# Kernel optimization log

Measured on AMD Instinct MI355X. Metric: run time of the kernel, lower is better.

## Reference

```python
import jax, jax.numpy as jnp
import numpy as np

BATCH = 256
SEQ = 2048        # sequences (in_features of each per-channel Linear)
C = 32            # input_size (number of independent channels/layers)
EMB = 2048        # embedding_dim (out_features)


def setup_inputs() -> dict:
    key = jax.random.key(0)
    kx, kw, kb = jax.random.split(key, 3)
    x = jax.random.normal(kx, (BATCH, SEQ, C), dtype=jnp.float32)
    # PyTorch nn.Linear init: U(-1/sqrt(fan_in), 1/sqrt(fan_in))
    bound = 1.0 / np.sqrt(SEQ)
    W = jax.random.uniform(kw, (C, SEQ, EMB), minval=-bound, maxval=bound, dtype=jnp.float32)
    b = jax.random.uniform(kb, (C, EMB), minval=-bound, maxval=bound, dtype=jnp.float32)
    return {"x": x, "W": W, "b": b}


def reference(x, W, b):
    # x: (B, S, C) -> transpose to (B, C, S); per-channel Linear + ReLU.
    # Grouped GEMM: out[b,c,e] = relu(sum_s x[b,s,c] * W[c,s,e] + b[c,e])
    xc = jnp.transpose(x, (0, 2, 1))                 # (B, C, S)
    out = jnp.einsum('bcs,cse->bce', xc, W) + b      # (B, C, E)
    return jax.nn.relu(out)
```

## Files before the change

kernel.cpp:

```cpp
#include <hip/hip_runtime.h>

#define BATCH 256
#define SEQ   2048
#define NC    32
#define EMB   2048
#define NT    32

typedef unsigned short ushort_t;
using f32x4  = __attribute__((ext_vector_type(4))) float;
using bf16x8 = __attribute__((ext_vector_type(8))) short;

using u32_gl = __attribute__((address_space(1))) const unsigned int;
using u32_ld = __attribute__((address_space(3))) unsigned int;

__device__ __forceinline__ unsigned short f2bf(float f) {
  unsigned int u = __float_as_uint(f);
  u += 0x7FFFu + ((u >> 16) & 1u);
  return (unsigned short)(u >> 16);
}

__global__ __launch_bounds__(256) void transpose_x_kernel(
    const float* __restrict__ x, ushort_t* __restrict__ xT) {
  __shared__ float tile[64][33];
  const int b  = blockIdx.x >> 5;
  const int st = blockIdx.x & 31;
  const int t  = threadIdx.x;
  const float* src = x + ((size_t)b * SEQ + (size_t)st * 64) * NC;
#pragma unroll
  for (int i = 0; i < 2; ++i) {
    int idx = t + i * 256;
    float4 v = reinterpret_cast<const float4*>(src)[idx];
    int s = idx >> 3;
    int c = (idx & 7) * 4;
    tile[s][c + 0] = v.x; tile[s][c + 1] = v.y;
    tile[s][c + 2] = v.z; tile[s][c + 3] = v.w;
  }
  __syncthreads();
  const int c  = t >> 3;
  const int si = (t & 7) * 8;
  unsigned int q[4];
#pragma unroll
  for (int p = 0; p < 4; ++p) {
    unsigned int h0 = f2bf(tile[si + 2 * p + 0][c]);
    unsigned int h1 = f2bf(tile[si + 2 * p + 1][c]);
    q[p] = h0 | (h1 << 16);
  }
  ushort_t* dst = xT + (size_t)c * (BATCH * SEQ) + (size_t)b * SEQ + st * 64 + si;
  *reinterpret_cast<uint4*>(dst) = make_uint4(q[0], q[1], q[2], q[3]);
}

template <int P>
__device__ __forceinline__ void gemm_iter(
    int t, const ushort_t* __restrict__ xTc, const float* __restrict__ Wc,
    char* AldsB, char* BldsB, f32x4 (&wv)[2][4], f32x4 (&acc)[4][4],
    int tid, int wr, int wc, int g, int lm, int e0) {
  const int srow4 = tid >> 5;
  const int e4    = tid & 31;

  asm volatile("s_waitcnt vmcnt(4)" ::: "memory");
#pragma unroll
  for (int i = 0; i < 4; ++i) {
    const int e_local = e4 * 4 + i;
    unsigned int q0 = (unsigned)f2bf(wv[P][0][i]) | ((unsigned)f2bf(wv[P][1][i]) << 16);
    unsigned int q1 = (unsigned)f2bf(wv[P][2][i]) | ((unsigned)f2bf(wv[P][3][i]) << 16);
    int byte = (e_local * 128 + srow4 * 8) ^ ((e_local & 7) << 4);
    *reinterpret_cast<uint2*>(BldsB + P * 16384 + byte) = make_uint2(q0, q1);
  }

  {
    const int tn = (t + 1) & (NT - 1);
    const float* wp = Wc + (size_t)(tn * 64 + srow4 * 4) * EMB + e0 + e4 * 4;
#pragma unroll
    for (int r = 0; r < 4; ++r)
      wv[P ^ 1][r] = *reinterpret_cast<const f32x4*>(wp + (size_t)r * EMB);
  }

  asm volatile("s_waitcnt lgkmcnt(0)" ::: "memory");
  __builtin_amdgcn_s_barrier();

  {
    const int s0n = ((t + 1) & (NT - 1)) * 64;
#pragma unroll
    for (int i = 0; i < 4; ++i) {
      int ch   = i * 512 + tid;
      int m    = ch >> 3;
      int slot = (ch & 7) ^ (m & 7);
      const ushort_t* src = xTc + (size_t)m * SEQ + s0n + slot * 8;
      __builtin_amdgcn_global_load_lds(
          (u32_gl*)src, (u32_ld*)(AldsB + (P ^ 1) * 32768 + ch * 16), 16, 0, 0);
    }
  }

  asm volatile("s_waitcnt vmcnt(8)" ::: "memory");
  __builtin_amdgcn_sched_barrier(0);

  __builtin_amdgcn_s_barrier();

#pragma unroll
  for (int ks = 0; ks < 2; ++ks) {
    bf16x8 af[4], bfr[4];
#pragma unroll
    for (int mi = 0; mi < 4; ++mi) {
      int m_local = wr * 64 + mi * 16 + lm;
      int byte = (m_local * 128 + (ks * 4 + g) * 16) ^ ((m_local & 7) << 4);
      af[mi] = *reinterpret_cast<const bf16x8*>(AldsB + P * 32768 + byte);
    }
#pragma unroll
    for (int ni = 0; ni < 4; ++ni) {
      int e_local = wc * 64 + ni * 16 + lm;
      int byte = (e_local * 128 + (ks * 4 + g) * 16) ^ ((e_local & 7) << 4);
      bfr[ni] = *reinterpret_cast<const bf16x8*>(BldsB + P * 16384 + byte);
    }
#pragma unroll
    for (int mi = 0; mi < 4; ++mi)
#pragma unroll
      for (int ni = 0; ni < 4; ++ni)
        acc[mi][ni] = __builtin_amdgcn_mfma_f32_16x16x32_bf16(
            af[mi], bfr[ni], acc[mi][ni], 0, 0, 0);
  }
}

__global__ __launch_bounds__(512, 2) void grouped_gemm_pipe(
    const ushort_t* __restrict__ xT,
    const float* __restrict__ W,
    const float* __restrict__ bias,
    float* __restrict__ out) {
  __shared__ ushort_t Alds[2][256 * 64];
  __shared__ ushort_t Blds[2][128 * 64];

  const int bid = (blockIdx.x & 7) * 64 + (blockIdx.x >> 3);
  const int c   = bid >> 4;
  const int et  = bid & 15;
  const int e0  = et * 128;

  const int tid  = threadIdx.x;
  const int w    = tid >> 6;
  const int wr   = w >> 1;
  const int wc   = w & 1;
  const int lane = tid & 63;
  const int g    = lane >> 4;
  const int lm   = lane & 15;

  const float* Wc = W + (size_t)c * SEQ * EMB;
  const ushort_t* xTc = xT + (size_t)c * (BATCH * SEQ);
  char* AldsB = (char*)&Alds[0][0];
  char* BldsB = (char*)&Blds[0][0];

  f32x4 wv[2][4];
  f32x4 acc[4][4];
#pragma unroll
  for (int i = 0; i < 4; ++i)
#pragma unroll
    for (int j = 0; j < 4; ++j) acc[i][j] = (f32x4){0.f, 0.f, 0.f, 0.f};

  {
    const int srow4 = tid >> 5;
    const int e4    = tid & 31;
    const float* wp = Wc + (size_t)(srow4 * 4) * EMB + e0 + e4 * 4;
#pragma unroll
    for (int r = 0; r < 4; ++r)
      wv[0][r] = *reinterpret_cast<const f32x4*>(wp + (size_t)r * EMB);
#pragma unroll
    for (int i = 0; i < 4; ++i) {
      int ch   = i * 512 + tid;
      int m    = ch >> 3;
      int slot = (ch & 7) ^ (m & 7);
      const ushort_t* src = xTc + (size_t)m * SEQ + slot * 8;
      __builtin_amdgcn_global_load_lds(
          (u32_gl*)src, (u32_ld*)(AldsB + ch * 16), 16, 0, 0);
    }
  }

  for (int t = 0; t < NT; t += 2) {
    gemm_iter<0>(t,     xTc, Wc, AldsB, BldsB, wv, acc, tid, wr, wc, g, lm, e0);
    gemm_iter<1>(t + 1, xTc, Wc, AldsB, BldsB, wv, acc, tid, wr, wc, g, lm, e0);
  }

  asm volatile("s_waitcnt vmcnt(0)" ::: "memory");

  const float* bc = bias + (size_t)c * EMB;
#pragma unroll
  for (int ni = 0; ni < 4; ++ni) {
    const int e = e0 + wc * 64 + ni * 16 + lm;
    const float bv = bc[e];
#pragma unroll
    for (int mi = 0; mi < 4; ++mi) {
      f32x4 a = acc[mi][ni];
      const int mbase = wr * 64 + mi * 16 + g * 4;
#pragma unroll
      for (int r = 0; r < 4; ++r) {
        float v = a[r] + bv;
        v = fmaxf(v, 0.f);
        out[((size_t)(mbase + r) * NC + c) * EMB + e] = v;
      }
    }
  }
}

__global__ __launch_bounds__(256, 2) void grouped_gemm_fallback(
    const float* __restrict__ x, const float* __restrict__ W,
    const float* __restrict__ bias, float* __restrict__ out) {
  __shared__ ushort_t Alds[128 * 64];
  __shared__ ushort_t Blds[128 * 64];
  const int bid = blockIdx.x;
  const int c   = bid >> 5;
  const int et  = (bid >> 1) & 15;
  const int bt  = bid & 1;
  const int b0  = bt * 128;
  const int e0  = et * 128;
  const int tid  = threadIdx.x;
  const int w    = tid >> 6;
  const int wr   = w >> 1;
  const int wc   = w & 1;
  const int lane = tid & 63;
  const int g    = lane >> 4;
  const int lm   = lane & 15;
  const float* Wc = W + (size_t)c * SEQ * EMB;
  const int srow8 = tid >> 5;
  const int e4    = tid & 31;
  f32x4 acc[4][4];
#pragma unroll
  for (int i = 0; i < 4; ++i)
#pragma unroll
    for (int j = 0; j < 4; ++j) acc[i][j] = (f32x4){0.f, 0.f, 0.f, 0.f};
  for (int s0 = 0; s0 < SEQ; s0 += 64) {
#pragma unroll
    for (int i = 0; i < 4; ++i) {
      int ch   = i * 256 + tid;
      int m    = ch >> 3;
      int slot = (ch & 7) ^ (m & 7);
      const float* src = x + (size_t)(b0 + m) * (SEQ * NC)
                           + (size_t)(s0 + slot * 8) * NC + c;
      unsigned int q[4];
#pragma unroll
      for (int p = 0; p < 4; ++p) {
        unsigned int h0 = f2bf(src[(2 * p + 0) * NC]);
        unsigned int h1 = f2bf(src[(2 * p + 1) * NC]);
        q[p] = h0 | (h1 << 16);
      }
      *reinterpret_cast<uint4*>((char*)&Alds[0] + ch * 16) =
          make_uint4(q[0], q[1], q[2], q[3]);
    }
    {
      const float* wp = Wc + (size_t)(s0 + srow8 * 8) * EMB + e0 + e4 * 4;
      f32x4 wvv[8];
#pragma unroll
      for (int r = 0; r < 8; ++r)
        wvv[r] = *reinterpret_cast<const f32x4*>(wp + (size_t)r * EMB);
#pragma unroll
      for (int i = 0; i < 4; ++i) {
        const int e_local = e4 * 4 + i;
        unsigned int q0 = (unsigned)f2bf(wvv[0][i]) | ((unsigned)f2bf(wvv[1][i]) << 16);
        unsigned int q1 = (unsigned)f2bf(wvv[2][i]) | ((unsigned)f2bf(wvv[3][i]) << 16);
        unsigned int q2 = (unsigned)f2bf(wvv[4][i]) | ((unsigned)f2bf(wvv[5][i]) << 16);
        unsigned int q3 = (unsigned)f2bf(wvv[6][i]) | ((unsigned)f2bf(wvv[7][i]) << 16);
        int byte = (e_local * 128 + srow8 * 16) ^ ((e_local & 7) << 4);
        *reinterpret_cast<uint4*>((char*)&Blds[0] + byte) =
            make_uint4(q0, q1, q2, q3);
      }
    }
    __syncthreads();
#pragma unroll
    for (int ks = 0; ks < 2; ++ks) {
      bf16x8 af[4], bfr[4];
#pragma unroll
      for (int mi = 0; mi < 4; ++mi) {
        int m_local = wr * 64 + mi * 16 + lm;
        int byte = (m_local * 128 + (ks * 4 + g) * 16) ^ ((m_local & 7) << 4);
        af[mi] = *reinterpret_cast<const bf16x8*>((const char*)&Alds[0] + byte);
      }
#pragma unroll
      for (int ni = 0; ni < 4; ++ni) {
        int e_local = wc * 64 + ni * 16 + lm;
        int byte = (e_local * 128 + (ks * 4 + g) * 16) ^ ((e_local & 7) << 4);
        bfr[ni] = *reinterpret_cast<const bf16x8*>((const char*)&Blds[0] + byte);
      }
#pragma unroll
      for (int mi = 0; mi < 4; ++mi)
#pragma unroll
        for (int ni = 0; ni < 4; ++ni)
          acc[mi][ni] = __builtin_amdgcn_mfma_f32_16x16x32_bf16(
              af[mi], bfr[ni], acc[mi][ni], 0, 0, 0);
    }
    __syncthreads();
  }
  const float* bc = bias + (size_t)c * EMB;
#pragma unroll
  for (int ni = 0; ni < 4; ++ni) {
    const int e = e0 + wc * 64 + ni * 16 + lm;
    const float bv = bc[e];
#pragma unroll
    for (int mi = 0; mi < 4; ++mi) {
      f32x4 a = acc[mi][ni];
      const int mbase = b0 + wr * 64 + mi * 16 + g * 4;
#pragma unroll
      for (int r = 0; r < 4; ++r) {
        float v = a[r] + bv;
        v = fmaxf(v, 0.f);
        out[((size_t)(mbase + r) * NC + c) * EMB + e] = v;
      }
    }
  }
}

extern "C" void kernel_launch(void* const* d_in, const int* in_sizes, int n_in,
                              void* d_out, int out_size, void* d_ws, size_t ws_size,
                              hipStream_t stream) {
  const float* x    = (const float*)d_in[0];
  const float* W    = (const float*)d_in[1];
  const float* bias = (const float*)d_in[2];
  float* out        = (float*)d_out;

  const size_t xT_bytes = (size_t)NC * BATCH * SEQ * sizeof(ushort_t);

  if (ws_size >= xT_bytes) {
    ushort_t* xT = (ushort_t*)d_ws;
    transpose_x_kernel<<<BATCH * (SEQ / 64), 256, 0, stream>>>(x, xT);
    grouped_gemm_pipe<<<NC * (EMB / 128), 512, 0, stream>>>(xT, W, bias, out);
  } else {
    grouped_gemm_fallback<<<NC * 2 * (EMB / 128), 256, 0, stream>>>(x, W, bias, out);
  }
}
```

Before: 158.5 us.

## Shrink GEMM tile to 256x64 with 4 waves and reorder W conversion after prefetch

The pipelined grouped GEMM now uses 64-wide E tiles with 256 threads (4 waves each covering 64 rows) instead of 128-wide tiles with 512 threads. This doubles the block count to 1024 and shrinks B LDS. The W fp32->bf16 conversion and LDS store now run after the next W prefetch is issued, with the waitcnt thresholds adjusted to match. In exchange, each block reloads the full 256x64 A tile for only half as many output columns, which doubles A traffic per FLOP.

```diff
diff --git a/kernel.cpp b/kernel.cpp
--- a/kernel.cpp
+++ b/kernel.cpp
@@ -13,10 +13,10 @@
 using u32_gl = __attribute__((address_space(1))) const unsigned int;
 using u32_ld = __attribute__((address_space(3))) unsigned int;
 
-__device__ __forceinline__ unsigned short f2bf(float f) {
+__device__ __forceinline__ unsigned int f2bf(float f) {
   unsigned int u = __float_as_uint(f);
   u += 0x7FFFu + ((u >> 16) & 1u);
-  return (unsigned short)(u >> 16);
+  return u >> 16;
 }
 
 __global__ __launch_bounds__(256) void transpose_x_kernel(
@@ -53,19 +53,9 @@
 __device__ __forceinline__ void gemm_iter(
     int t, const ushort_t* __restrict__ xTc, const float* __restrict__ Wc,
     char* AldsB, char* BldsB, f32x4 (&wv)[2][4], f32x4 (&acc)[4][4],
-    int tid, int wr, int wc, int g, int lm, int e0) {
-  const int srow4 = tid >> 5;
-  const int e4    = tid & 31;
-
-  asm volatile("s_waitcnt vmcnt(4)" ::: "memory");
-#pragma unroll
-  for (int i = 0; i < 4; ++i) {
-    const int e_local = e4 * 4 + i;
-    unsigned int q0 = (unsigned)f2bf(wv[P][0][i]) | ((unsigned)f2bf(wv[P][1][i]) << 16);
-    unsigned int q1 = (unsigned)f2bf(wv[P][2][i]) | ((unsigned)f2bf(wv[P][3][i]) << 16);
-    int byte = (e_local * 128 + srow4 * 8) ^ ((e_local & 7) << 4);
-    *reinterpret_cast<uint2*>(BldsB + P * 16384 + byte) = make_uint2(q0, q1);
-  }
+    int tid, int wr, int g, int lm, int e0) {
+  const int srow4 = tid >> 4;
+  const int e4    = tid & 15;
 
   {
     const int tn = (t + 1) & (NT - 1);
@@ -75,14 +65,24 @@
       wv[P ^ 1][r] = *reinterpret_cast<const f32x4*>(wp + (size_t)r * EMB);
   }
 
+  asm volatile("s_waitcnt vmcnt(12)" ::: "memory");
+#pragma unroll
+  for (int i = 0; i < 4; ++i) {
+    const int e_local = e4 * 4 + i;
+    unsigned int q0 = f2bf(wv[P][0][i]) | (f2bf(wv[P][1][i]) << 16);
+    unsigned int q1 = f2bf(wv[P][2][i]) | (f2bf(wv[P][3][i]) << 16);
+    int byte = (e_local * 128 + srow4 * 8) ^ ((e_local & 7) << 4);
+    *reinterpret_cast<uint2*>(BldsB + P * 8192 + byte) = make_uint2(q0, q1);
+  }
+
   asm volatile("s_waitcnt lgkmcnt(0)" ::: "memory");
   __builtin_amdgcn_s_barrier();
 
   {
     const int s0n = ((t + 1) & (NT - 1)) * 64;
 #pragma unroll
-    for (int i = 0; i < 4; ++i) {
-      int ch   = i * 512 + tid;
+    for (int i = 0; i < 8; ++i) {
+      int ch   = i * 256 + tid;
       int m    = ch >> 3;
       int slot = (ch & 7) ^ (m & 7);
       const ushort_t* src = xTc + (size_t)m * SEQ + s0n + slot * 8;
@@ -91,7 +91,7 @@
     }
   }
 
-  asm volatile("s_waitcnt vmcnt(8)" ::: "memory");
+  asm volatile("s_waitcnt vmcnt(12)" ::: "memory");
   __builtin_amdgcn_sched_barrier(0);
 
   __builtin_amdgcn_s_barrier();
@@ -107,9 +107,9 @@
     }
 #pragma unroll
     for (int ni = 0; ni < 4; ++ni) {
-      int e_local = wc * 64 + ni * 16 + lm;
+      int e_local = ni * 16 + lm;
       int byte = (e_local * 128 + (ks * 4 + g) * 16) ^ ((e_local & 7) << 4);
-      bfr[ni] = *reinterpret_cast<const bf16x8*>(BldsB + P * 16384 + byte);
+      bfr[ni] = *reinterpret_cast<const bf16x8*>(BldsB + P * 8192 + byte);
     }
 #pragma unroll
     for (int mi = 0; mi < 4; ++mi)
@@ -120,23 +120,21 @@
   }
 }
 
-__global__ __launch_bounds__(512, 2) void grouped_gemm_pipe(
+__global__ __launch_bounds__(256, 2) void grouped_gemm_pipe(
     const ushort_t* __restrict__ xT,
     const float* __restrict__ W,
     const float* __restrict__ bias,
     float* __restrict__ out) {
   __shared__ ushort_t Alds[2][256 * 64];
-  __shared__ ushort_t Blds[2][128 * 64];
-
-  const int bid = (blockIdx.x & 7) * 64 + (blockIdx.x >> 3);
-  const int c   = bid >> 4;
-  const int et  = bid & 15;
-  const int e0  = et * 128;
+  __shared__ ushort_t Blds[2][64 * 64];
+
+  const int bid = (blockIdx.x & 7) * 128 + (blockIdx.x >> 3);
+  const int c   = bid >> 5;
+  const int et  = bid & 31;
+  const int e0  = et * 64;
 
   const int tid  = threadIdx.x;
-  const int w    = tid >> 6;
-  const int wr   = w >> 1;
-  const int wc   = w & 1;
+  const int wr   = tid >> 6;
   const int lane = tid & 63;
   const int g    = lane >> 4;
   const int lm   = lane & 15;
@@ -154,15 +152,15 @@
     for (int j = 0; j < 4; ++j) acc[i][j] = (f32x4){0.f, 0.f, 0.f, 0.f};
 
   {
-    const int srow4 = tid >> 5;
-    const int e4    = tid & 31;
+    const int srow4 = tid >> 4;
+    const int e4    = tid & 15;
     const float* wp = Wc + (size_t)(srow4 * 4) * EMB + e0 + e4 * 4;
 #pragma unroll
     for (int r = 0; r < 4; ++r)
       wv[0][r] = *reinterpret_cast<const f32x4*>(wp + (size_t)r * EMB);
 #pragma unroll
-    for (int i = 0; i < 4; ++i) {
-      int ch   = i * 512 + tid;
+    for (int i = 0; i < 8; ++i) {
+      int ch   = i * 256 + tid;
       int m    = ch >> 3;
       int slot = (ch & 7) ^ (m & 7);
       const ushort_t* src = xTc + (size_t)m * SEQ + slot * 8;
@@ -172,8 +170,8 @@
   }
 
   for (int t = 0; t < NT; t += 2) {
-    gemm_iter<0>(t,     xTc, Wc, AldsB, BldsB, wv, acc, tid, wr, wc, g, lm, e0);
-    gemm_iter<1>(t + 1, xTc, Wc, AldsB, BldsB, wv, acc, tid, wr, wc, g, lm, e0);
+    gemm_iter<0>(t,     xTc, Wc, AldsB, BldsB, wv, acc, tid, wr, g, lm, e0);
+    gemm_iter<1>(t + 1, xTc, Wc, AldsB, BldsB, wv, acc, tid, wr, g, lm, e0);
   }
 
   asm volatile("s_waitcnt vmcnt(0)" ::: "memory");
@@ -181,7 +179,7 @@
   const float* bc = bias + (size_t)c * EMB;
 #pragma unroll
   for (int ni = 0; ni < 4; ++ni) {
-    const int e = e0 + wc * 64 + ni * 16 + lm;
+    const int e = e0 + ni * 16 + lm;
     const float bv = bc[e];
 #pragma unroll
     for (int mi = 0; mi < 4; ++mi) {
@@ -250,10 +248,10 @@
 #pragma unroll
       for (int i = 0; i < 4; ++i) {
         const int e_local = e4 * 4 + i;
-        unsigned int q0 = (unsigned)f2bf(wvv[0][i]) | ((unsigned)f2bf(wvv[1][i]) << 16);
-        unsigned int q1 = (unsigned)f2bf(wvv[2][i]) | ((unsigned)f2bf(wvv[3][i]) << 16);
-        unsigned int q2 = (unsigned)f2bf(wvv[4][i]) | ((unsigned)f2bf(wvv[5][i]) << 16);
-        unsigned int q3 = (unsigned)f2bf(wvv[6][i]) | ((unsigned)f2bf(wvv[7][i]) << 16);
+        unsigned int q0 = f2bf(wvv[0][i]) | (f2bf(wvv[1][i]) << 16);
+        unsigned int q1 = f2bf(wvv[2][i]) | (f2bf(wvv[3][i]) << 16);
+        unsigned int q2 = f2bf(wvv[4][i]) | (f2bf(wvv[5][i]) << 16);
+        unsigned int q3 = f2bf(wvv[6][i]) | (f2bf(wvv[7][i]) << 16);
         int byte = (e_local * 128 + srow8 * 16) ^ ((e_local & 7) << 4);
         *reinterpret_cast<uint4*>((char*)&Blds[0] + byte) =
             make_uint4(q0, q1, q2, q3);
@@ -316,7 +314,7 @@
   if (ws_size >= xT_bytes) {
     ushort_t* xT = (ushort_t*)d_ws;
     transpose_x_kernel<<<BATCH * (SEQ / 64), 256, 0, stream>>>(x, xT);
-    grouped_gemm_pipe<<<NC * (EMB / 128), 512, 0, stream>>>(xT, W, bias, out);
+    grouped_gemm_pipe<<<NC * (EMB / 64), 256, 0, stream>>>(xT, W, bias, out);
   } else {
     grouped_gemm_fallback<<<NC * 2 * (EMB / 128), 256, 0, stream>>>(x, W, bias, out);
   }
```

New measurement: 174.4 us. +10.0%, slower.

## Deepen GEMM pipeline to four stages with K=32 tiles

Applied to the files above, without the earlier changes.

Restructures the grouped GEMM main loop from a 2-stage pipeline with 64-wide K tiles to a 4-stage ring of 32-wide K tiles. Activation tiles are prefetched two steps ahead and W fp32 loads four steps ahead, with a new paired-row swizzled LDS layout. The aim is to hide more global-memory latency behind the MFMA work. In exchange there are twice as many barriers per K, the register budget changes, and launch bounds drop to one block per SIMD group, which may reduce occupancy.

```diff
diff --git a/kernel.cpp b/kernel.cpp
--- a/kernel.cpp
+++ b/kernel.cpp
@@ -4,20 +4,23 @@
 #define SEQ   2048
 #define NC    32
 #define EMB   2048
-#define NT    32
+#define NT    64
 
 typedef unsigned short ushort_t;
+using f32x2  = __attribute__((ext_vector_type(2))) float;
 using f32x4  = __attribute__((ext_vector_type(4))) float;
 using bf16x8 = __attribute__((ext_vector_type(8))) short;
 
 using u32_gl = __attribute__((address_space(1))) const unsigned int;
 using u32_ld = __attribute__((address_space(3))) unsigned int;
 
-__device__ __forceinline__ unsigned short f2bf(float f) {
+__device__ __forceinline__ unsigned int f2bf(float f) {
   unsigned int u = __float_as_uint(f);
   u += 0x7FFFu + ((u >> 16) & 1u);
-  return (unsigned short)(u >> 16);
-}
+  return u >> 16;
+}
+
+#define SB() __builtin_amdgcn_sched_barrier(0)
 
 __global__ __launch_bounds__(256) void transpose_x_kernel(
     const float* __restrict__ x, ushort_t* __restrict__ xT) {
@@ -49,67 +52,74 @@
   *reinterpret_cast<uint4*>(dst) = make_uint4(q[0], q[1], q[2], q[3]);
 }
 
-template <int P>
-__device__ __forceinline__ void gemm_iter(
+template <int Q>
+__device__ __forceinline__ void giter(
     int t, const ushort_t* __restrict__ xTc, const float* __restrict__ Wc,
-    char* AldsB, char* BldsB, f32x4 (&wv)[2][4], f32x4 (&acc)[4][4],
+    char* Alds, char* Blds, f32x2 (&wv)[4][4], f32x4 (&acc)[4][4],
     int tid, int wr, int wc, int g, int lm, int e0) {
-  const int srow4 = tid >> 5;
-  const int e4    = tid & 31;
-
-  asm volatile("s_waitcnt vmcnt(4)" ::: "memory");
-#pragma unroll
-  for (int i = 0; i < 4; ++i) {
-    const int e_local = e4 * 4 + i;
-    unsigned int q0 = (unsigned)f2bf(wv[P][0][i]) | ((unsigned)f2bf(wv[P][1][i]) << 16);
-    unsigned int q1 = (unsigned)f2bf(wv[P][2][i]) | ((unsigned)f2bf(wv[P][3][i]) << 16);
-    int byte = (e_local * 128 + srow4 * 8) ^ ((e_local & 7) << 4);
-    *reinterpret_cast<uint2*>(BldsB + P * 16384 + byte) = make_uint2(q0, q1);
-  }
-
-  {
-    const int tn = (t + 1) & (NT - 1);
-    const float* wp = Wc + (size_t)(tn * 64 + srow4 * 4) * EMB + e0 + e4 * 4;
-#pragma unroll
-    for (int r = 0; r < 4; ++r)
-      wv[P ^ 1][r] = *reinterpret_cast<const f32x4*>(wp + (size_t)r * EMB);
-  }
-
+  constexpr int QA = (Q + 2) & 3;
+
+  {
+    const int s0n = ((t + 2) & (NT - 1)) * 32;
+#pragma unroll
+    for (int i = 0; i < 2; ++i) {
+      int ch = i * 512 + tid;
+      int r  = ch >> 3;
+      int sp = (ch & 7) ^ (r & 7);
+      int m  = 2 * r + (sp >> 2);
+      int s8 = sp & 3;
+      const ushort_t* src = xTc + (size_t)m * SEQ + s0n + s8 * 8;
+      __builtin_amdgcn_global_load_lds(
+          (u32_gl*)src, (u32_ld*)(Alds + QA * 16384 + ch * 16), 16, 0, 0);
+    }
+  }
+  SB();
+
+  {
+    const int s0w = ((t + 4) & (NT - 1)) * 32;
+    const float* wp = Wc + (size_t)(s0w + (tid >> 6) * 4) * EMB + e0 + (tid & 63) * 2;
+#pragma unroll
+    for (int j = 0; j < 4; ++j)
+      wv[Q][j] = *reinterpret_cast<const f32x2*>(wp + (size_t)j * EMB);
+  }
+  SB();
+
+  asm volatile("s_waitcnt vmcnt(12)" ::: "memory");
+  SB();
+
+  {
+    const int e2 = tid & 63;
+    const int s4 = tid >> 6;
+#pragma unroll
+    for (int d = 0; d < 2; ++d) {
+      const int e = e2 * 2 + d;
+      unsigned int lo = f2bf(wv[QA][0][d]) | (f2bf(wv[QA][1][d]) << 16);
+      unsigned int hi = f2bf(wv[QA][2][d]) | (f2bf(wv[QA][3][d]) << 16);
+      int sig  = (((e & 1) << 2) + (s4 >> 1)) ^ ((e >> 1) & 7);
+      int byte = (e >> 1) * 128 + sig * 16 + (s4 & 1) * 8;
+      *reinterpret_cast<uint2*>(Blds + QA * 8192 + byte) = make_uint2(lo, hi);
+    }
+  }
   asm volatile("s_waitcnt lgkmcnt(0)" ::: "memory");
+  SB();
+
   __builtin_amdgcn_s_barrier();
 
   {
-    const int s0n = ((t + 1) & (NT - 1)) * 64;
-#pragma unroll
-    for (int i = 0; i < 4; ++i) {
-      int ch   = i * 512 + tid;
-      int m    = ch >> 3;
-      int slot = (ch & 7) ^ (m & 7);
-      const ushort_t* src = xTc + (size_t)m * SEQ + s0n + slot * 8;
-      __builtin_amdgcn_global_load_lds(
-          (u32_gl*)src, (u32_ld*)(AldsB + (P ^ 1) * 32768 + ch * 16), 16, 0, 0);
-    }
-  }
-
-  asm volatile("s_waitcnt vmcnt(8)" ::: "memory");
-  __builtin_amdgcn_sched_barrier(0);
-
-  __builtin_amdgcn_s_barrier();
-
-#pragma unroll
-  for (int ks = 0; ks < 2; ++ks) {
     bf16x8 af[4], bfr[4];
 #pragma unroll
     for (int mi = 0; mi < 4; ++mi) {
-      int m_local = wr * 64 + mi * 16 + lm;
-      int byte = (m_local * 128 + (ks * 4 + g) * 16) ^ ((m_local & 7) << 4);
-      af[mi] = *reinterpret_cast<const bf16x8*>(AldsB + P * 32768 + byte);
+      int m  = wr * 64 + mi * 16 + lm;
+      int r  = m >> 1;
+      int sig = (((m & 1) << 2) + g) ^ (r & 7);
+      af[mi] = *reinterpret_cast<const bf16x8*>(Alds + Q * 16384 + r * 128 + sig * 16);
     }
 #pragma unroll
     for (int ni = 0; ni < 4; ++ni) {
-      int e_local = wc * 64 + ni * 16 + lm;
-      int byte = (e_local * 128 + (ks * 4 + g) * 16) ^ ((e_local & 7) << 4);
-      bfr[ni] = *reinterpret_cast<const bf16x8*>(BldsB + P * 16384 + byte);
+      int e  = wc * 64 + ni * 16 + lm;
+      int r  = e >> 1;
+      int sig = (((e & 1) << 2) + g) ^ (r & 7);
+      bfr[ni] = *reinterpret_cast<const bf16x8*>(Blds + Q * 8192 + r * 128 + sig * 16);
     }
 #pragma unroll
     for (int mi = 0; mi < 4; ++mi)
@@ -120,13 +130,13 @@
   }
 }
 
-__global__ __launch_bounds__(512, 2) void grouped_gemm_pipe(
+__global__ __launch_bounds__(512, 1) void grouped_gemm_pipe(
     const ushort_t* __restrict__ xT,
     const float* __restrict__ W,
     const float* __restrict__ bias,
     float* __restrict__ out) {
-  __shared__ ushort_t Alds[2][256 * 64];
-  __shared__ ushort_t Blds[2][128 * 64];
+  __shared__ ushort_t AldsU[4][256 * 32];
+  __shared__ ushort_t BldsU[4][128 * 32];
 
   const int bid = (blockIdx.x & 7) * 64 + (blockIdx.x >> 3);
   const int c   = bid >> 4;
@@ -143,10 +153,10 @@
 
   const float* Wc = W + (size_t)c * SEQ * EMB;
   const ushort_t* xTc = xT + (size_t)c * (BATCH * SEQ);
-  char* AldsB = (char*)&Alds[0][0];
-  char* BldsB = (char*)&Blds[0][0];
-
-  f32x4 wv[2][4];
+  char* Alds = (char*)&AldsU[0][0];
+  char* Blds = (char*)&BldsU[0][0];
+
+  f32x2 wv[4][4];
   f32x4 acc[4][4];
 #pragma unroll
   for (int i = 0; i < 4; ++i)
@@ -154,26 +164,79 @@
     for (int j = 0; j < 4; ++j) acc[i][j] = (f32x4){0.f, 0.f, 0.f, 0.f};
 
   {
-    const int srow4 = tid >> 5;
-    const int e4    = tid & 31;
-    const float* wp = Wc + (size_t)(srow4 * 4) * EMB + e0 + e4 * 4;
-#pragma unroll
-    for (int r = 0; r < 4; ++r)
-      wv[0][r] = *reinterpret_cast<const f32x4*>(wp + (size_t)r * EMB);
-#pragma unroll
-    for (int i = 0; i < 4; ++i) {
-      int ch   = i * 512 + tid;
-      int m    = ch >> 3;
-      int slot = (ch & 7) ^ (m & 7);
-      const ushort_t* src = xTc + (size_t)m * SEQ + slot * 8;
+    const int s4 = tid >> 6;
+    const int e2 = tid & 63;
+    const float* wpb = Wc + (size_t)(s4 * 4) * EMB + e0 + e2 * 2;
+#pragma unroll
+    for (int j = 0; j < 4; ++j)
+      wv[0][j] = *reinterpret_cast<const f32x2*>(wpb + (size_t)j * EMB);
+    SB();
+#pragma unroll
+    for (int j = 0; j < 4; ++j)
+      wv[1][j] = *reinterpret_cast<const f32x2*>(wpb + (size_t)(32 + j) * EMB);
+    SB();
+#pragma unroll
+    for (int i = 0; i < 2; ++i) {
+      int ch = i * 512 + tid;
+      int r  = ch >> 3;
+      int sp = (ch & 7) ^ (r & 7);
+      int m  = 2 * r + (sp >> 2);
+      const ushort_t* src = xTc + (size_t)m * SEQ + (sp & 3) * 8;
       __builtin_amdgcn_global_load_lds(
-          (u32_gl*)src, (u32_ld*)(AldsB + ch * 16), 16, 0, 0);
-    }
-  }
-
-  for (int t = 0; t < NT; t += 2) {
-    gemm_iter<0>(t,     xTc, Wc, AldsB, BldsB, wv, acc, tid, wr, wc, g, lm, e0);
-    gemm_iter<1>(t + 1, xTc, Wc, AldsB, BldsB, wv, acc, tid, wr, wc, g, lm, e0);
+          (u32_gl*)src, (u32_ld*)(Alds + ch * 16), 16, 0, 0);
+    }
+    SB();
+#pragma unroll
+    for (int j = 0; j < 4; ++j)
+      wv[2][j] = *reinterpret_cast<const f32x2*>(wpb + (size_t)(64 + j) * EMB);
+    SB();
+#pragma unroll
+    for (int i = 0; i < 2; ++i) {
+      int ch = i * 512 + tid;
+      int r  = ch >> 3;
+      int sp = (ch & 7) ^ (r & 7);
+      int m  = 2 * r + (sp >> 2);
+      const ushort_t* src = xTc + (size_t)m * SEQ + 32 + (sp & 3) * 8;
+      __builtin_amdgcn_global_load_lds(
+          (u32_gl*)src, (u32_ld*)(Alds + 16384 + ch * 16), 16, 0, 0);
+    }
+    SB();
+#pragma unroll
+    for (int j = 0; j < 4; ++j)
+      wv[3][j] = *reinterpret_cast<const f32x2*>(wpb + (size_t)(96 + j) * EMB);
+    SB();
+
+    asm volatile("s_waitcnt vmcnt(16)" ::: "memory");
+    SB();
+#pragma unroll
+    for (int d = 0; d < 2; ++d) {
+      const int e = e2 * 2 + d;
+      unsigned int lo = f2bf(wv[0][0][d]) | (f2bf(wv[0][1][d]) << 16);
+      unsigned int hi = f2bf(wv[0][2][d]) | (f2bf(wv[0][3][d]) << 16);
+      int sig  = (((e & 1) << 2) + (s4 >> 1)) ^ ((e >> 1) & 7);
+      int byte = (e >> 1) * 128 + sig * 16 + (s4 & 1) * 8;
+      *reinterpret_cast<uint2*>(Blds + byte) = make_uint2(lo, hi);
+    }
+    SB();
+    asm volatile("s_waitcnt vmcnt(12)" ::: "memory");
+    SB();
+#pragma unroll
+    for (int d = 0; d < 2; ++d) {
+      const int e = e2 * 2 + d;
+      unsigned int lo = f2bf(wv[1][0][d]) | (f2bf(wv[1][1][d]) << 16);
+      unsigned int hi = f2bf(wv[1][2][d]) | (f2bf(wv[1][3][d]) << 16);
+      int sig  = (((e & 1) << 2) + (s4 >> 1)) ^ ((e >> 1) & 7);
+      int byte = (e >> 1) * 128 + sig * 16 + (s4 & 1) * 8;
+      *reinterpret_cast<uint2*>(Blds + 8192 + byte) = make_uint2(lo, hi);
+    }
+    SB();
+  }
+
+  for (int t = 0; t < NT; t += 4) {
+    giter<0>(t,     xTc, Wc, Alds, Blds, wv, acc, tid, wr, wc, g, lm, e0);
+    giter<1>(t + 1, xTc, Wc, Alds, Blds, wv, acc, tid, wr, wc, g, lm, e0);
+    giter<2>(t + 2, xTc, Wc, Alds, Blds, wv, acc, tid, wr, wc, g, lm, e0);
+    giter<3>(t + 3, xTc, Wc, Alds, Blds, wv, acc, tid, wr, wc, g, lm, e0);
   }
 
   asm volatile("s_waitcnt vmcnt(0)" ::: "memory");
@@ -250,10 +313,10 @@
 #pragma unroll
       for (int i = 0; i < 4; ++i) {
         const int e_local = e4 * 4 + i;
-        unsigned int q0 = (unsigned)f2bf(wvv[0][i]) | ((unsigned)f2bf(wvv[1][i]) << 16);
-        unsigned int q1 = (unsigned)f2bf(wvv[2][i]) | ((unsigned)f2bf(wvv[3][i]) << 16);
-        unsigned int q2 = (unsigned)f2bf(wvv[4][i]) | ((unsigned)f2bf(wvv[5][i]) << 16);
-        unsigned int q3 = (unsigned)f2bf(wvv[6][i]) | ((unsigned)f2bf(wvv[7][i]) << 16);
+        unsigned int q0 = f2bf(wvv[0][i]) | (f2bf(wvv[1][i]) << 16);
+        unsigned int q1 = f2bf(wvv[2][i]) | (f2bf(wvv[3][i]) << 16);
+        unsigned int q2 = f2bf(wvv[4][i]) | (f2bf(wvv[5][i]) << 16);
+        unsigned int q3 = f2bf(wvv[6][i]) | (f2bf(wvv[7][i]) << 16);
         int byte = (e_local * 128 + srow8 * 16) ^ ((e_local & 7) << 4);
         *reinterpret_cast<uint4*>((char*)&Blds[0] + byte) =
             make_uint4(q0, q1, q2, q3);
```

Result: slower. 184.2 us (+16.2%).

## Deepen GEMM prefetch to distance two with triple-buffered A tile

Applied to the files above, without the earlier changes.

The main loop now fetches the W register tile and the xT LDS tile two K-steps ahead instead of one. The A operand gets a third LDS buffer, indexed cyclically, and the loop is unrolled by six with two tail iterations. The s_waitcnt vmcnt thresholds are raised and schedule barriers added to match, so more global memory latency can hide behind MFMA work. In exchange it costs extra LDS (128KB per block), more in-flight registers, and a few wasted wrap-around loads at the end of the loop.

```diff
diff --git a/kernel.cpp b/kernel.cpp
--- a/kernel.cpp
+++ b/kernel.cpp
@@ -13,11 +13,13 @@
 using u32_gl = __attribute__((address_space(1))) const unsigned int;
 using u32_ld = __attribute__((address_space(3))) unsigned int;
 
-__device__ __forceinline__ unsigned short f2bf(float f) {
+__device__ __forceinline__ unsigned int f2bf(float f) {
   unsigned int u = __float_as_uint(f);
   u += 0x7FFFu + ((u >> 16) & 1u);
-  return (unsigned short)(u >> 16);
-}
+  return u >> 16;
+}
+
+#define SB() __builtin_amdgcn_sched_barrier(0)
 
 __global__ __launch_bounds__(256) void transpose_x_kernel(
     const float* __restrict__ x, ushort_t* __restrict__ xT) {
@@ -49,37 +51,40 @@
   *reinterpret_cast<uint4*>(dst) = make_uint4(q[0], q[1], q[2], q[3]);
 }
 
-template <int P>
+template <int PB, int Q3>
 __device__ __forceinline__ void gemm_iter(
     int t, const ushort_t* __restrict__ xTc, const float* __restrict__ Wc,
-    char* AldsB, char* BldsB, f32x4 (&wv)[2][4], f32x4 (&acc)[4][4],
+    char* Alds, char* Blds, f32x4 (&wv)[2][4], f32x4 (&acc)[4][4],
     int tid, int wr, int wc, int g, int lm, int e0) {
+  constexpr int QS = (Q3 + 2) % 3;
   const int srow4 = tid >> 5;
   const int e4    = tid & 31;
 
-  asm volatile("s_waitcnt vmcnt(4)" ::: "memory");
+  asm volatile("s_waitcnt vmcnt(12)" ::: "memory");
+
 #pragma unroll
   for (int i = 0; i < 4; ++i) {
     const int e_local = e4 * 4 + i;
-    unsigned int q0 = (unsigned)f2bf(wv[P][0][i]) | ((unsigned)f2bf(wv[P][1][i]) << 16);
-    unsigned int q1 = (unsigned)f2bf(wv[P][2][i]) | ((unsigned)f2bf(wv[P][3][i]) << 16);
+    unsigned int q0 = f2bf(wv[PB][0][i]) | (f2bf(wv[PB][1][i]) << 16);
+    unsigned int q1 = f2bf(wv[PB][2][i]) | (f2bf(wv[PB][3][i]) << 16);
     int byte = (e_local * 128 + srow4 * 8) ^ ((e_local & 7) << 4);
-    *reinterpret_cast<uint2*>(BldsB + P * 16384 + byte) = make_uint2(q0, q1);
+    *reinterpret_cast<uint2*>(Blds + PB * 16384 + byte) = make_uint2(q0, q1);
   }
 
   {
-    const int tn = (t + 1) & (NT - 1);
+    const int tn = (t + 2) & (NT - 1);
     const float* wp = Wc + (size_t)(tn * 64 + srow4 * 4) * EMB + e0 + e4 * 4;
 #pragma unroll
     for (int r = 0; r < 4; ++r)
-      wv[P ^ 1][r] = *reinterpret_cast<const f32x4*>(wp + (size_t)r * EMB);
-  }
+      wv[PB][r] = *reinterpret_cast<const f32x4*>(wp + (size_t)r * EMB);
+  }
+  SB();
 
   asm volatile("s_waitcnt lgkmcnt(0)" ::: "memory");
   __builtin_amdgcn_s_barrier();
 
   {
-    const int s0n = ((t + 1) & (NT - 1)) * 64;
+    const int s0n = ((t + 2) & (NT - 1)) * 64;
 #pragma unroll
     for (int i = 0; i < 4; ++i) {
       int ch   = i * 512 + tid;
@@ -87,12 +92,12 @@
       int slot = (ch & 7) ^ (m & 7);
       const ushort_t* src = xTc + (size_t)m * SEQ + s0n + slot * 8;
       __builtin_amdgcn_global_load_lds(
-          (u32_gl*)src, (u32_ld*)(AldsB + (P ^ 1) * 32768 + ch * 16), 16, 0, 0);
-    }
-  }
-
-  asm volatile("s_waitcnt vmcnt(8)" ::: "memory");
-  __builtin_amdgcn_sched_barrier(0);
+          (u32_gl*)src, (u32_ld*)(Alds + QS * 32768 + ch * 16), 16, 0, 0);
+    }
+  }
+
+  asm volatile("s_waitcnt vmcnt(16)" ::: "memory");
+  SB();
 
   __builtin_amdgcn_s_barrier();
 
@@ -103,13 +108,13 @@
     for (int mi = 0; mi < 4; ++mi) {
       int m_local = wr * 64 + mi * 16 + lm;
       int byte = (m_local * 128 + (ks * 4 + g) * 16) ^ ((m_local & 7) << 4);
-      af[mi] = *reinterpret_cast<const bf16x8*>(AldsB + P * 32768 + byte);
+      af[mi] = *reinterpret_cast<const bf16x8*>(Alds + Q3 * 32768 + byte);
     }
 #pragma unroll
     for (int ni = 0; ni < 4; ++ni) {
       int e_local = wc * 64 + ni * 16 + lm;
       int byte = (e_local * 128 + (ks * 4 + g) * 16) ^ ((e_local & 7) << 4);
-      bfr[ni] = *reinterpret_cast<const bf16x8*>(BldsB + P * 16384 + byte);
+      bfr[ni] = *reinterpret_cast<const bf16x8*>(Blds + PB * 16384 + byte);
     }
 #pragma unroll
     for (int mi = 0; mi < 4; ++mi)
@@ -125,8 +130,8 @@
     const float* __restrict__ W,
     const float* __restrict__ bias,
     float* __restrict__ out) {
-  __shared__ ushort_t Alds[2][256 * 64];
-  __shared__ ushort_t Blds[2][128 * 64];
+  __shared__ ushort_t AldsU[3][256 * 64];
+  __shared__ ushort_t BldsU[2][128 * 64];
 
   const int bid = (blockIdx.x & 7) * 64 + (blockIdx.x >> 3);
   const int c   = bid >> 4;
@@ -143,8 +148,8 @@
 
   const float* Wc = W + (size_t)c * SEQ * EMB;
   const ushort_t* xTc = xT + (size_t)c * (BATCH * SEQ);
-  char* AldsB = (char*)&Alds[0][0];
-  char* BldsB = (char*)&Blds[0][0];
+  char* Alds = (char*)&AldsU[0][0];
+  char* Blds = (char*)&BldsU[0][0];
 
   f32x4 wv[2][4];
   f32x4 acc[4][4];
@@ -160,6 +165,7 @@
 #pragma unroll
     for (int r = 0; r < 4; ++r)
       wv[0][r] = *reinterpret_cast<const f32x4*>(wp + (size_t)r * EMB);
+    SB();
 #pragma unroll
     for (int i = 0; i < 4; ++i) {
       int ch   = i * 512 + tid;
@@ -167,14 +173,35 @@
       int slot = (ch & 7) ^ (m & 7);
       const ushort_t* src = xTc + (size_t)m * SEQ + slot * 8;
       __builtin_amdgcn_global_load_lds(
-          (u32_gl*)src, (u32_ld*)(AldsB + ch * 16), 16, 0, 0);
-    }
-  }
-
-  for (int t = 0; t < NT; t += 2) {
-    gemm_iter<0>(t,     xTc, Wc, AldsB, BldsB, wv, acc, tid, wr, wc, g, lm, e0);
-    gemm_iter<1>(t + 1, xTc, Wc, AldsB, BldsB, wv, acc, tid, wr, wc, g, lm, e0);
-  }
+          (u32_gl*)src, (u32_ld*)(Alds + ch * 16), 16, 0, 0);
+    }
+    SB();
+#pragma unroll
+    for (int r = 0; r < 4; ++r)
+      wv[1][r] = *reinterpret_cast<const f32x4*>(wp + (size_t)(64 + r) * EMB);
+    SB();
+#pragma unroll
+    for (int i = 0; i < 4; ++i) {
+      int ch   = i * 512 + tid;
+      int m    = ch >> 3;
+      int slot = (ch & 7) ^ (m & 7);
+      const ushort_t* src = xTc + (size_t)m * SEQ + 64 + slot * 8;
+      __builtin_amdgcn_global_load_lds(
+          (u32_gl*)src, (u32_ld*)(Alds + 32768 + ch * 16), 16, 0, 0);
+    }
+    SB();
+  }
+
+  for (int t = 0; t < 30; t += 6) {
+    gemm_iter<0, 0>(t,     xTc, Wc, Alds, Blds, wv, acc, tid, wr, wc, g, lm, e0);
+    gemm_iter<1, 1>(t + 1, xTc, Wc, Alds, Blds, wv, acc, tid, wr, wc, g, lm, e0);
+    gemm_iter<0, 2>(t + 2, xTc, Wc, Alds, Blds, wv, acc, tid, wr, wc, g, lm, e0);
+    gemm_iter<1, 0>(t + 3, xTc, Wc, Alds, Blds, wv, acc, tid, wr, wc, g, lm, e0);
+    gemm_iter<0, 1>(t + 4, xTc, Wc, Alds, Blds, wv, acc, tid, wr, wc, g, lm, e0);
+    gemm_iter<1, 2>(t + 5, xTc, Wc, Alds, Blds, wv, acc, tid, wr, wc, g, lm, e0);
+  }
+  gemm_iter<0, 0>(30, xTc, Wc, Alds, Blds, wv, acc, tid, wr, wc, g, lm, e0);
+  gemm_iter<1, 1>(31, xTc, Wc, Alds, Blds, wv, acc, tid, wr, wc, g, lm, e0);
 
   asm volatile("s_waitcnt vmcnt(0)" ::: "memory");
 
@@ -250,10 +277,10 @@
 #pragma unroll
       for (int i = 0; i < 4; ++i) {
         const int e_local = e4 * 4 + i;
-        unsigned int q0 = (unsigned)f2bf(wvv[0][i]) | ((unsigned)f2bf(wvv[1][i]) << 16);
-        unsigned int q1 = (unsigned)f2bf(wvv[2][i]) | ((unsigned)f2bf(wvv[3][i]) << 16);
-        unsigned int q2 = (unsigned)f2bf(wvv[4][i]) | ((unsigned)f2bf(wvv[5][i]) << 16);
-        unsigned int q3 = (unsigned)f2bf(wvv[6][i]) | ((unsigned)f2bf(wvv[7][i]) << 16);
+        unsigned int q0 = f2bf(wvv[0][i]) | (f2bf(wvv[1][i]) << 16);
+        unsigned int q1 = f2bf(wvv[2][i]) | (f2bf(wvv[3][i]) << 16);
+        unsigned int q2 = f2bf(wvv[4][i]) | (f2bf(wvv[5][i]) << 16);
+        unsigned int q3 = f2bf(wvv[6][i]) | (f2bf(wvv[7][i]) << 16);
         int byte = (e_local * 128 + srow8 * 16) ^ ((e_local & 7) << 4);
         *reinterpret_cast<uint4*>((char*)&Blds[0] + byte) =
             make_uint4(q0, q1, q2, q3);
```

New measurement: 159.9 us. About the same (+0.8%).
